# Kernel optimization log

Measured on AMD Instinct MI355X. Metric: run time of the kernel, lower is better.

The kernel has to match this reference:

```python
import jax, jax.numpy as jnp
import numpy as np

IN_CH = 64
OUT_CH = 64
K = 5
PAD = 2
B, H, W = 16, 128, 128


def _build_buffers():
    # Mirrors the torch __init__ geometry construction exactly.
    r = (K - 1) // 2
    x = np.arange(-r, r + 1)
    X = np.stack(np.meshgrid(x, x, indexing='ij'), -1).astype(np.float32)  # (K,K,2)
    R = np.sqrt((X ** 2).sum(-1))                                          # (K,K)
    with np.errstate(divide='ignore', invalid='ignore'):
        Xhat = X / R[..., None]
    Xhat[R == 0] = 0.0
    Xhat = np.transpose(Xhat, (2, 0, 1))                 # (2,K,K)
    XX = Xhat[None, :] * Xhat[:, None]                   # (2,2,K,K) outer product
    XX = np.tile(XX, (OUT_CH, IN_CH, 1, 1))              # (2*out, 2*in, K, K)
    rs, inds = np.unique(R, return_inverse=True)
    inds = inds.reshape(K, K).astype(np.int32)
    indsxx = inds - 1
    indsxx[indsxx == -1] = 0                              # r=0 bin has no xx term (masked by XX=0 there)
    identity = np.tile(np.eye(2, dtype=np.float32), (OUT_CH, IN_CH))[..., None, None]  # (2*out,2*in,1,1)
    return XX.astype(np.float32), identity, indsxx, inds, len(rs)


def setup_inputs() -> dict:
    XX, identity, indsxx, indsid, L = _build_buffers()
    key = jax.random.key(0)
    k1, k2, k3 = jax.random.split(key, 3)
    scale = np.float32(1.0 / np.sqrt(3 * IN_CH * 2))
    return {
        'x': jax.random.normal(k1, (B, 2 * IN_CH, H, W), jnp.float32),
        'weightsxx': jax.random.normal(k2, (OUT_CH, IN_CH, L - 1), jnp.float32) * scale,
        'weightsidentity': jax.random.normal(k3, (OUT_CH, IN_CH, L), jnp.float32) * scale,
        'XhatXhat': jnp.asarray(XX),
        'identity': jnp.asarray(identity),
        'indsxx': jnp.asarray(indsxx),
        'indsidentity': jnp.asarray(indsid),
        'padding': PAD,
    }


def _build_kernel(weightsxx, weightsidentity, XhatXhat, identity, indsxx, indsidentity):
    # repeat_interleave(.,2,axis) == jnp.repeat(.,2,axis); then radial gather over (K,K)
    cxx = jnp.repeat(jnp.repeat(weightsxx, 2, axis=0), 2, axis=1)[..., indsxx] * XhatXhat
    cid = jnp.repeat(jnp.repeat(weightsidentity, 2, axis=0), 2, axis=1)[..., indsidentity] * identity
    return cxx + cid  # (2*out, 2*in, K, K)


def reference(x, weightsxx, weightsidentity, XhatXhat, identity, indsxx, indsidentity, padding):
    c = _build_kernel(weightsxx, weightsidentity, XhatXhat, identity, indsxx, indsidentity)
    xp = jnp.pad(x, ((0, 0), (0, 0), (padding, padding), (padding, padding)))
    return jax.lax.conv_general_dilated(
        xp, c, window_strides=(1, 1), padding='VALID',
        dimension_numbers=('NCHW', 'OIHW', 'NCHW'))
```

## Files before the change

### kernel.cpp

```cpp
#include <hip/hip_runtime.h>
#include <hip/hip_bf16.h>

typedef __bf16        bf16x8 __attribute__((ext_vector_type(8)));
typedef float         f32x16 __attribute__((ext_vector_type(16)));
typedef unsigned int  u32x4  __attribute__((ext_vector_type(4)));
typedef unsigned int   u32;
typedef unsigned short u16;

__device__ __forceinline__ u16 f32_to_bf16(float f) {
    u32 u = __builtin_bit_cast(u32, f);
    u = (u + 0x7FFFu + ((u >> 16) & 1u)) >> 16;
    return (u16)u;
}
__device__ __forceinline__ u32 pack2bf(float a, float b) {
    return (u32)f32_to_bf16(a) | ((u32)f32_to_bf16(b) << 16);
}

__global__ void build_c(const float* __restrict__ wxx,
                        const float* __restrict__ wid,
                        const float* __restrict__ XX,
                        const float* __restrict__ ident,
                        const int*   __restrict__ indsxx,
                        const int*   __restrict__ indsid,
                        u16*         __restrict__ cb)
{
    int idx = blockIdx.x * 256 + threadIdx.x;
    if (idx >= 25 * 128 * 128) return;
    int b = idx & 127;
    int a = (idx >> 7) & 127;
    int t = idx >> 14;
    int w2 = (a >> 1) * 64 + (b >> 1);
    float v = wxx[w2 * 5 + indsxx[t]] * XX[(a * 128 + b) * 25 + t]
            + ident[a * 128 + b]      * wid[w2 * 6 + indsid[t]];
    cb[idx] = f32_to_bf16(v);
}

__global__ void __launch_bounds__(512, 2)
conv_mfma(const float* __restrict__ x,
          const u16*   __restrict__ cb,
          float*       __restrict__ out)
{
    __shared__ u32x4 lds4[2 * 4224];

    const int tid    = threadIdx.x;
    const int lane   = tid & 63;
    const int wv     = tid >> 6;
    const int wave_m = wv & 1;
    const int wave_n = wv >> 1;
    const int l31    = lane & 31;
    const int h2     = lane >> 5;

    const int bid  = blockIdx.x;
    const int sbid = (bid & 7) * 64 + (bid >> 3);
    const int bb   = sbid >> 5;
    const int h0   = (sbid & 31) << 2;

    const int wc     = tid & 127;
    const int icq    = tid >> 7;
    const int wp_st  = wc + 2;
    const int st_idx = (wp_st << 2) + (icq ^ ((wp_st >> 1) & 3));

    if (tid < 256) {
        const int wtab[4] = {0, 1, 130, 131};
        int b  = tid >> 7;
        int t  = tid & 127;
        int r  = t >> 4, wq = (t >> 2) & 3, q = t & 3;
        u32x4 z = {0, 0, 0, 0};
        lds4[b * 4224 + r * 528 + (wtab[wq] << 2) + q] = z;
    }

    f32x16 acc[2][4];
    #pragma unroll
    for (int i = 0; i < 2; ++i)
        #pragma unroll
        for (int j = 0; j < 4; ++j)
            #pragma unroll
            for (int k = 0; k < 16; ++k) acc[i][j][k] = 0.f;

    float pf[8][8];
    const float* xb = x + (bb * 128 + icq * 8) * 16384 + wc;

    auto ISSUE = [&](int ich) {
        const float* bx = xb + ich * 32 * 16384;
        #pragma unroll
        for (int r = 0; r < 8; ++r) {
            int hp = h0 - 2 + r;
            if ((unsigned)hp < 128u) {
                const float* px = bx + hp * 128;
                #pragma unroll
                for (int k = 0; k < 8; ++k) pf[r][k] = px[k * 16384];
            } else {
                #pragma unroll
                for (int k = 0; k < 8; ++k) pf[r][k] = 0.f;
            }
        }
    };

    auto WRITE = [&](u32x4* buf) {
        #pragma unroll
        for (int r = 0; r < 8; ++r) {
            u32x4 v;
            v[0] = pack2bf(pf[r][0], pf[r][1]);
            v[1] = pack2bf(pf[r][2], pf[r][3]);
            v[2] = pack2bf(pf[r][4], pf[r][5]);
            v[3] = pack2bf(pf[r][6], pf[r][7]);
            buf[r * 528 + st_idx] = v;
        }
    };

    auto COMPUTE = [&](const u32x4* buf, int ich) {
        const u16* cbt = cb + (wave_m * 64 + l31) * 128 + ich * 32 + h2 * 8;
        #pragma unroll
        for (int kh = 0; kh < 5; ++kh) {
            const int rbase = (wave_n + kh) * 528;
            #pragma unroll
            for (int kw = 0; kw < 5; ++kw) {
                const u16* cp = cbt + (kh * 5 + kw) * 16384;
                const bf16x8 a0k0 = *reinterpret_cast<const bf16x8*>(cp);
                const bf16x8 a0k1 = *reinterpret_cast<const bf16x8*>(cp + 16);
                const bf16x8 a1k0 = *reinterpret_cast<const bf16x8*>(cp + 4096);
                const bf16x8 a1k1 = *reinterpret_cast<const bf16x8*>(cp + 4096 + 16);
                const int wsum = kw + l31;
                const int vsw  = (wsum >> 1) & 3;
                const int cb0  = rbase + (wsum << 2);
                const int i0   = cb0 + (h2 ^ vsw);
                const int i1   = cb0 + ((2 + h2) ^ vsw);
                #pragma unroll
                for (int nf = 0; nf < 4; ++nf) {
                    const bf16x8 b0 = __builtin_bit_cast(bf16x8, buf[i0 + nf * 128]);
                    const bf16x8 b1 = __builtin_bit_cast(bf16x8, buf[i1 + nf * 128]);
                    acc[0][nf] = __builtin_amdgcn_mfma_f32_32x32x16_bf16(a0k0, b0, acc[0][nf], 0, 0, 0);
                    acc[0][nf] = __builtin_amdgcn_mfma_f32_32x32x16_bf16(a0k1, b1, acc[0][nf], 0, 0, 0);
                    acc[1][nf] = __builtin_amdgcn_mfma_f32_32x32x16_bf16(a1k0, b0, acc[1][nf], 0, 0, 0);
                    acc[1][nf] = __builtin_amdgcn_mfma_f32_32x32x16_bf16(a1k1, b1, acc[1][nf], 0, 0, 0);
                }
            }
        }
    };

    ISSUE(0);
    WRITE(lds4);
    __syncthreads();

    #pragma unroll 1
    for (int ich = 0; ich < 4; ++ich) {
        if (ich < 3) ISSUE(ich + 1);
        COMPUTE(lds4 + (ich & 1) * 4224, ich);
        if (ich < 3) WRITE(lds4 + ((ich + 1) & 1) * 4224);
        __syncthreads();
    }

    const int h = h0 + wave_n;
    float* ob = out + ((size_t)(bb * 128 + wave_m * 64) * 128 + h) * 128 + l31;
    #pragma unroll
    for (int mf = 0; mf < 2; ++mf)
        #pragma unroll
        for (int reg = 0; reg < 16; ++reg) {
            const int oc = mf * 32 + (reg & 3) + ((reg >> 2) << 3) + (h2 << 2);
            float* op = ob + (size_t)oc * 16384;
            #pragma unroll
            for (int nf = 0; nf < 4; ++nf)
                op[nf * 32] = acc[mf][nf][reg];
        }
}

extern "C" void kernel_launch(void* const* d_in, const int* in_sizes, int n_in,
                              void* d_out, int out_size, void* d_ws, size_t ws_size,
                              hipStream_t stream)
{
    const float* x    = (const float*)d_in[0];
    const float* wxx  = (const float*)d_in[1];
    const float* wi   = (const float*)d_in[2];
    const float* XX   = (const float*)d_in[3];
    const float* iden = (const float*)d_in[4];
    const int*   ixx  = (const int*)d_in[5];
    const int*   iid  = (const int*)d_in[6];

    u16* cbuf = (u16*)d_ws;

    build_c<<<1600, 256, 0, stream>>>(wxx, wi, XX, iden, ixx, iid, cbuf);
    conv_mfma<<<512, 512, 0, stream>>>(x, cbuf, (float*)d_out);
}
```

Measured before the change: 232.2 us.

## Remap waves to width strips and reuse each LDS B fragment across kernel rows

Each wave now covers a 32-pixel width strip across all 4 output rows instead of one output row across 128 pixels. Inside the kw loop it loads the A fragments for all 5 kh taps, then reads each of the 8 padded input rows from LDS once and applies it to every output row it feeds. This cuts LDS reads, and A is fetched once per (kw,kk) instead of per (kh,kw). The change also drops the occupancy hint to 1 block per CU so the larger A register set fits, and raises wave priority around the MFMA bursts.

New measurement: 311.4 us. 34.1% more time.

```diff
diff --git a/kernel.cpp b/kernel.cpp
--- a/kernel.cpp
+++ b/kernel.cpp
@@ -35,7 +35,7 @@
     cb[idx] = f32_to_bf16(v);
 }
 
-__global__ void __launch_bounds__(512, 2)
+__global__ void __launch_bounds__(512, 1)
 conv_mfma(const float* __restrict__ x,
           const u16*   __restrict__ cb,
           float*       __restrict__ out)
@@ -46,7 +46,7 @@
     const int lane   = tid & 63;
     const int wv     = tid >> 6;
     const int wave_m = wv & 1;
-    const int wave_n = wv >> 1;
+    const int wave_w = wv >> 1;
     const int l31    = lane & 31;
     const int h2     = lane >> 5;
 
@@ -62,11 +62,11 @@
 
     if (tid < 256) {
         const int wtab[4] = {0, 1, 130, 131};
-        int b  = tid >> 7;
-        int t  = tid & 127;
+        int bsel = tid >> 7;
+        int t    = tid & 127;
         int r  = t >> 4, wq = (t >> 2) & 3, q = t & 3;
         u32x4 z = {0, 0, 0, 0};
-        lds4[b * 4224 + r * 528 + (wtab[wq] << 2) + q] = z;
+        lds4[bsel * 4224 + r * 528 + (wtab[wq] << 2) + q] = z;
     }
 
     f32x16 acc[2][4];
@@ -109,31 +109,37 @@
     };
 
     auto COMPUTE = [&](const u32x4* buf, int ich) {
-        const u16* cbt = cb + (wave_m * 64 + l31) * 128 + ich * 32 + h2 * 8;
+        const u16* cbA   = cb + (wave_m * 64 + l31) * 128 + ich * 32 + h2 * 8;
+        const int  wbase = wave_w * 32 + l31;
         #pragma unroll
-        for (int kh = 0; kh < 5; ++kh) {
-            const int rbase = (wave_n + kh) * 528;
+        for (int kw = 0; kw < 5; ++kw) {
+            const int wp  = wbase + kw;
+            const int vsw = (wp >> 1) & 3;
+            const int cb0 = wp << 2;
             #pragma unroll
-            for (int kw = 0; kw < 5; ++kw) {
-                const u16* cp = cbt + (kh * 5 + kw) * 16384;
-                const bf16x8 a0k0 = *reinterpret_cast<const bf16x8*>(cp);
-                const bf16x8 a0k1 = *reinterpret_cast<const bf16x8*>(cp + 16);
-                const bf16x8 a1k0 = *reinterpret_cast<const bf16x8*>(cp + 4096);
-                const bf16x8 a1k1 = *reinterpret_cast<const bf16x8*>(cp + 4096 + 16);
-                const int wsum = kw + l31;
-                const int vsw  = (wsum >> 1) & 3;
-                const int cb0  = rbase + (wsum << 2);
-                const int i0   = cb0 + (h2 ^ vsw);
-                const int i1   = cb0 + ((2 + h2) ^ vsw);
+            for (int kk = 0; kk < 2; ++kk) {
+                bf16x8 A[5][2];
                 #pragma unroll
-                for (int nf = 0; nf < 4; ++nf) {
-                    const bf16x8 b0 = __builtin_bit_cast(bf16x8, buf[i0 + nf * 128]);
-                    const bf16x8 b1 = __builtin_bit_cast(bf16x8, buf[i1 + nf * 128]);
-                    acc[0][nf] = __builtin_amdgcn_mfma_f32_32x32x16_bf16(a0k0, b0, acc[0][nf], 0, 0, 0);
-                    acc[0][nf] = __builtin_amdgcn_mfma_f32_32x32x16_bf16(a0k1, b1, acc[0][nf], 0, 0, 0);
-                    acc[1][nf] = __builtin_amdgcn_mfma_f32_32x32x16_bf16(a1k0, b0, acc[1][nf], 0, 0, 0);
-                    acc[1][nf] = __builtin_amdgcn_mfma_f32_32x32x16_bf16(a1k1, b1, acc[1][nf], 0, 0, 0);
+                for (int kh = 0; kh < 5; ++kh) {
+                    const u16* cp = cbA + (kh * 5 + kw) * 16384 + kk * 16;
+                    A[kh][0] = *reinterpret_cast<const bf16x8*>(cp);
+                    A[kh][1] = *reinterpret_cast<const bf16x8*>(cp + 4096);
                 }
+                const int cidx = cb0 + ((kk * 2 + h2) ^ vsw);
+                __builtin_amdgcn_s_setprio(1);
+                #pragma unroll
+                for (int rp = 0; rp < 8; ++rp) {
+                    const bf16x8 b = __builtin_bit_cast(bf16x8, buf[rp * 528 + cidx]);
+                    #pragma unroll
+                    for (int kh = 0; kh < 5; ++kh) {
+                        const int n = rp - kh;
+                        if (0 <= n && n < 4) {
+                            acc[0][n] = __builtin_amdgcn_mfma_f32_32x32x16_bf16(A[kh][0], b, acc[0][n], 0, 0, 0);
+                            acc[1][n] = __builtin_amdgcn_mfma_f32_32x32x16_bf16(A[kh][1], b, acc[1][n], 0, 0, 0);
+                        }
+                    }
+                }
+                __builtin_amdgcn_s_setprio(0);
             }
         }
     };
@@ -150,17 +156,16 @@
         __syncthreads();
     }
 
-    const int h = h0 + wave_n;
-    float* ob = out + ((size_t)(bb * 128 + wave_m * 64) * 128 + h) * 128 + l31;
+    const int wpix = wave_w * 32 + l31;
     #pragma unroll
-    for (int mf = 0; mf < 2; ++mf)
+    for (int m = 0; m < 2; ++m)
         #pragma unroll
         for (int reg = 0; reg < 16; ++reg) {
-            const int oc = mf * 32 + (reg & 3) + ((reg >> 2) << 3) + (h2 << 2);
-            float* op = ob + (size_t)oc * 16384;
+            const int oc = wave_m * 64 + m * 32 + (reg & 3) + ((reg >> 2) << 3) + (h2 << 2);
+            float* op = out + ((size_t)(bb * 128 + oc) * 128 + h0) * 128 + wpix;
             #pragma unroll
-            for (int nf = 0; nf < 4; ++nf)
-                op[nf * 32] = acc[mf][nf][reg];
+            for (int n = 0; n < 4; ++n)
+                op[n * 128] = acc[m][n][reg];
         }
 }
 
```
